# Optimization experiments

Hardware: AMD Instinct MI355X
Metric: run time of the kernel (lower is better)

Reference implementation:

```python
import jax, jax.numpy as jnp
import numpy as np

FACTOR = 5  # routing softmax power


def setup_inputs() -> dict:
    key = jax.random.key(0)
    kq, kk, kv = jax.random.split(key, 3)
    B, L, S, H, E, D = 2, 2048, 2048, 16, 64, 64
    queries = jax.random.normal(kq, (B, L, H, E), dtype=jnp.float32)
    keys = jax.random.normal(kk, (B, S, H, E), dtype=jnp.float32)
    values = jax.random.normal(kv, (B, S, H, D), dtype=jnp.float32)
    return {"queries": queries, "keys": keys, "values": values}


def reference(queries, keys, values):
    # NOTE: original computes scale = 1/sqrt(E) but never applies it; faithful.
    # Original computes the same unscaled QK^T twice; compute once and reuse.
    scores = jnp.einsum('blhe,bshe->bhls', queries, keys)  # [B,H,L,S]
    dense = jax.nn.softmax(scores, axis=-1)
    routing = dense ** FACTOR  # softmax(scores)**factor == routing_scores
    combined = (routing + dense) * 0.5
    sparse = combined / jnp.sum(combined, axis=-1, keepdims=True)
    V = jnp.einsum('bhls,bshd->blhd', sparse, values)  # [B,L,H,D]
    return V
```

## Files before the change

kernel.cpp:

```cpp
#include <hip/hip_runtime.h>
#include <math.h>


typedef _Float16 h8 __attribute__((ext_vector_type(8)));
typedef float f4 __attribute__((ext_vector_type(4)));
typedef float f16v __attribute__((ext_vector_type(16)));
typedef unsigned int u4v __attribute__((ext_vector_type(4)));

constexpr int Sc = 2048, Hc = 16;
constexpr int KB = 64, NT = Sc / KB;
constexpr float LOG2E = 1.4426950408889634f;

__device__ __forceinline__ f16v mm32(h8 a, h8 b, f16v c) {
  return __builtin_amdgcn_mfma_f32_32x32x16_f16(a, b, c, 0, 0, 0);
}
__device__ __forceinline__ unsigned pku(float a, float b) {
  return __builtin_bit_cast(unsigned, __builtin_amdgcn_cvt_pkrtz(a, b));
}

__global__ __launch_bounds__(256, 2) void dsa_mfma(
    const float* __restrict__ Q, const float* __restrict__ K,
    const float* __restrict__ V, float* __restrict__ O) {
  __shared__ __align__(16) _Float16 Ks[2][64 * 64];
  __shared__ __align__(16) _Float16 Vts[2][64 * 64];

  const int tid = threadIdx.x;
  const int w = tid >> 6, lane = tid & 63, lm = lane & 31, hi = lane >> 5;
  const int swz = (lm & 7) << 3;

  const int blk = blockIdx.x;
  const int ww = (blk & 7) * 64 + (blk >> 3);
  const int qtb = ww & 15, bh = ww >> 4;
  const int b = bh >> 4, h = bh & 15;

  const size_t base = ((size_t)b * Sc * Hc + h) * 64;
  const float* Qb = Q + base;
  const float* Kb = K + base;
  const float* Vb = V + base;
  const int q0 = qtb * 128 + w * 32;

  h8 qf[4];
#pragma unroll
  for (int s = 0; s < 4; ++s) {
    const float* p = Qb + (size_t)(q0 + lm) * 1024 + s * 16 + hi * 8;
    f4 a = *(const f4*)p, c = *(const f4*)(p + 4);
#pragma unroll
    for (int i = 0; i < 4; ++i) {
      qf[s][i] = (_Float16)(a[i] * LOG2E);
      qf[s][4 + i] = (_Float16)(c[i] * LOG2E);
    }
  }

  f16v O1[2] = {}, O5[2] = {};
  float mr = -INFINITY, S1 = 0.f, S5 = 0.f;

  f4 kf[4];
  float vreg[2][8];
  const int krow = tid & 63, kq = tid >> 6;
  const int vd = tid & 63, vo0 = (tid >> 6) * 2;

  auto LOADK = [&](int k0) {
#pragma unroll
    for (int j = 0; j < 4; ++j)
      kf[j] = *(const f4*)(Kb + (size_t)(k0 + krow) * 1024 + kq * 16 + 4 * j);
  };
  auto LOADV = [&](int k0) {
#pragma unroll
    for (int i = 0; i < 2; ++i) {
      const float* p = Vb + (size_t)(k0 + (vo0 + i) * 8) * 1024 + vd;
#pragma unroll
      for (int j = 0; j < 8; ++j) vreg[i][j] = p[(size_t)j * 1024];
    }
  };
  auto STORE = [&](int buf) {
#pragma unroll
    for (int i = 0; i < 2; ++i) {
      u4v wv = {pku(kf[2 * i][0], kf[2 * i][1]), pku(kf[2 * i][2], kf[2 * i][3]),
                pku(kf[2 * i + 1][0], kf[2 * i + 1][1]), pku(kf[2 * i + 1][2], kf[2 * i + 1][3])};
      int col = (kq * 16 + 8 * i) ^ ((krow & 7) << 3);
      *(h8*)&Ks[buf][krow * 64 + col] = __builtin_bit_cast(h8, wv);
    }
#pragma unroll
    for (int i = 0; i < 2; ++i) {
      u4v wv = {pku(vreg[i][0], vreg[i][1]), pku(vreg[i][2], vreg[i][3]),
                pku(vreg[i][4], vreg[i][5]), pku(vreg[i][6], vreg[i][7])};
      int col = ((vo0 + i) * 8) ^ ((vd & 7) << 3);
      *(h8*)&Vts[buf][vd * 64 + col] = __builtin_bit_cast(h8, wv);
    }
  };

  LOADK(0);
  LOADV(0);
  STORE(0);
  LOADK(KB);
  LOADV(KB);
  __syncthreads();

#pragma unroll 1
  for (int t = 0; t < NT; ++t) {
    const int cur = t & 1;
    if (t + 1 < NT) STORE(cur ^ 1);
    if (t + 2 < NT) {
      LOADK((t + 2) * KB);
      LOADV((t + 2) * KB);
    }

    f16v sc[2] = {};
    __builtin_amdgcn_s_setprio(1);
#pragma unroll
    for (int s = 0; s < 4; ++s) {
      h8 a0 = *(const h8*)&Ks[cur][lm * 64 + ((s * 16 + hi * 8) ^ swz)];
      h8 a1 = *(const h8*)&Ks[cur][(32 + lm) * 64 + ((s * 16 + hi * 8) ^ swz)];
      sc[0] = mm32(a0, qf[s], sc[0]);
      sc[1] = mm32(a1, qf[s], sc[1]);
    }
    __builtin_amdgcn_s_setprio(0);

    float tm = -INFINITY;
#pragma unroll
    for (int kh = 0; kh < 2; ++kh)
#pragma unroll
      for (int r = 0; r < 16; ++r) tm = fmaxf(tm, sc[kh][r]);
    tm = fmaxf(tm, __shfl_xor(tm, 32));
    if (__any(tm > mr)) {
      float nm = fmaxf(mr, tm);
      float f = __builtin_amdgcn_exp2f(mr - nm);
      float f2 = f * f, f5 = f2 * f2 * f;
      mr = nm;
      S1 *= f;
      S5 *= f5;
#pragma unroll
      for (int dt = 0; dt < 2; ++dt) {
        O1[dt] *= f;
        O5[dt] *= f5;
      }
    }

    float t1 = 0.f, t5 = 0.f;
#pragma unroll
    for (int s = 0; s < 4; ++s) {
      const int kh = s >> 1, s8 = (s & 1) * 8;
      float e[8], e5[8];
#pragma unroll
      for (int j = 0; j < 8; ++j) {
        e[j] = __builtin_amdgcn_exp2f(sc[kh][s8 + j] - mr);
        float e2 = e[j] * e[j];
        e5[j] = e2 * e2 * e[j];
        t1 += e[j];
        t5 += e5[j];
      }
      auto rA = __builtin_amdgcn_permlane32_swap(pku(e[0], e[1]), pku(e[4], e[5]), false, false);
      auto rB = __builtin_amdgcn_permlane32_swap(pku(e[2], e[3]), pku(e[6], e[7]), false, false);
      u4v bwE = {(unsigned)rA[0], (unsigned)rB[0], (unsigned)rA[1], (unsigned)rB[1]};
      h8 bE = __builtin_bit_cast(h8, bwE);
      auto rC = __builtin_amdgcn_permlane32_swap(pku(e5[0], e5[1]), pku(e5[4], e5[5]), false, false);
      auto rD = __builtin_amdgcn_permlane32_swap(pku(e5[2], e5[3]), pku(e5[6], e5[7]), false, false);
      u4v bw5 = {(unsigned)rC[0], (unsigned)rD[0], (unsigned)rC[1], (unsigned)rD[1]};
      h8 b5 = __builtin_bit_cast(h8, bw5);

      h8 v0 = *(const h8*)&Vts[cur][lm * 64 + ((s * 16 + hi * 8) ^ swz)];
      h8 v1 = *(const h8*)&Vts[cur][(32 + lm) * 64 + ((s * 16 + hi * 8) ^ swz)];
      __builtin_amdgcn_s_setprio(1);
      O1[0] = mm32(v0, bE, O1[0]);
      O1[1] = mm32(v1, bE, O1[1]);
      O5[0] = mm32(v0, b5, O5[0]);
      O5[1] = mm32(v1, b5, O5[1]);
      __builtin_amdgcn_s_setprio(0);
    }
    t1 += __shfl_xor(t1, 32);
    t5 += __shfl_xor(t5, 32);
    S1 += t1;
    S5 += t5;

    __syncthreads();
  }

  const float z = S1, z2 = z * z, z4 = z2 * z2;
  const float inv = 1.0f / (S5 + z4 * S1);
#pragma unroll
  for (int dt = 0; dt < 2; ++dt)
#pragma unroll
    for (int i = 0; i < 4; ++i) {
      f4 o;
#pragma unroll
      for (int j = 0; j < 4; ++j)
        o[j] = (O5[dt][4 * i + j] + z4 * O1[dt][4 * i + j]) * inv;
      *(f4*)(O + base + (size_t)(q0 + lm) * 1024 + dt * 32 + 8 * i + 4 * hi) = o;
    }
}

extern "C" void kernel_launch(void* const* d_in, const int* in_sizes, int n_in,
                              void* d_out, int out_size, void* d_ws, size_t ws_size,
                              hipStream_t stream) {
  const float* q = (const float*)d_in[0];
  const float* k = (const float*)d_in[1];
  const float* v = (const float*)d_in[2];
  float* o = (float*)d_out;
  dsa_mfma<<<dim3(512), dim3(256), 0, stream>>>(q, k, v, o);
}
```

Before: 93.15 us.

## Compute row sums via MFMA with ones and fifth power in packed fp16

Replaces the scalar per-element accumulation of the exp and exp^5 row sums with extra MFMA instructions that multiply a ones vector by the probability fragments. The fifth power is now computed after packing, as fp16 vector multiplies, so only one set of permlane swaps is needed. The running-max reduction becomes a tree reduction. This removes VALU work and shuffles but adds two MFMAs per sub-step and computes the fifth power in fp16 instead of fp32, which can underflow or lose precision.

New measurement: 91.35 us. About the same (-1.9%).

```diff
diff --git a/kernel.cpp b/kernel.cpp
--- a/kernel.cpp
+++ b/kernel.cpp
@@ -50,9 +50,13 @@
       qf[s][4 + i] = (_Float16)(c[i] * LOG2E);
     }
   }
+  h8 ones;
+#pragma unroll
+  for (int i = 0; i < 8; ++i) ones[i] = (_Float16)1.0f;
 
   f16v O1[2] = {}, O5[2] = {};
-  float mr = -INFINITY, S1 = 0.f, S5 = 0.f;
+  f16v S1a = {}, S5a = {};
+  float mr = -INFINITY;
 
   f4 kf[4];
   float vreg[2][8];
@@ -116,19 +120,21 @@
     }
     __builtin_amdgcn_s_setprio(0);
 
-    float tm = -INFINITY;
+    float m16[16];
 #pragma unroll
-    for (int kh = 0; kh < 2; ++kh)
+    for (int r = 0; r < 16; ++r) m16[r] = fmaxf(sc[0][r], sc[1][r]);
 #pragma unroll
-      for (int r = 0; r < 16; ++r) tm = fmaxf(tm, sc[kh][r]);
-    tm = fmaxf(tm, __shfl_xor(tm, 32));
+    for (int d = 8; d >= 1; d >>= 1)
+#pragma unroll
+      for (int r = 0; r < d; ++r) m16[r] = fmaxf(m16[r], m16[r + d]);
+    float tm = fmaxf(m16[0], __shfl_xor(m16[0], 32));
     if (__any(tm > mr)) {
       float nm = fmaxf(mr, tm);
       float f = __builtin_amdgcn_exp2f(mr - nm);
       float f2 = f * f, f5 = f2 * f2 * f;
       mr = nm;
-      S1 *= f;
-      S5 *= f5;
+      S1a *= f;
+      S5a *= f5;
 #pragma unroll
       for (int dt = 0; dt < 2; ++dt) {
         O1[dt] *= f;
@@ -136,47 +142,35 @@
       }
     }
 
-    float t1 = 0.f, t5 = 0.f;
 #pragma unroll
     for (int s = 0; s < 4; ++s) {
       const int kh = s >> 1, s8 = (s & 1) * 8;
-      float e[8], e5[8];
+      float e[8];
 #pragma unroll
-      for (int j = 0; j < 8; ++j) {
-        e[j] = __builtin_amdgcn_exp2f(sc[kh][s8 + j] - mr);
-        float e2 = e[j] * e[j];
-        e5[j] = e2 * e2 * e[j];
-        t1 += e[j];
-        t5 += e5[j];
-      }
+      for (int j = 0; j < 8; ++j) e[j] = __builtin_amdgcn_exp2f(sc[kh][s8 + j] - mr);
       auto rA = __builtin_amdgcn_permlane32_swap(pku(e[0], e[1]), pku(e[4], e[5]), false, false);
       auto rB = __builtin_amdgcn_permlane32_swap(pku(e[2], e[3]), pku(e[6], e[7]), false, false);
       u4v bwE = {(unsigned)rA[0], (unsigned)rB[0], (unsigned)rA[1], (unsigned)rB[1]};
       h8 bE = __builtin_bit_cast(h8, bwE);
-      auto rC = __builtin_amdgcn_permlane32_swap(pku(e5[0], e5[1]), pku(e5[4], e5[5]), false, false);
-      auto rD = __builtin_amdgcn_permlane32_swap(pku(e5[2], e5[3]), pku(e5[6], e5[7]), false, false);
-      u4v bw5 = {(unsigned)rC[0], (unsigned)rD[0], (unsigned)rC[1], (unsigned)rD[1]};
-      h8 b5 = __builtin_bit_cast(h8, bw5);
+      h8 b2 = bE * bE, b4 = b2 * b2, b5 = b4 * bE;
 
       h8 v0 = *(const h8*)&Vts[cur][lm * 64 + ((s * 16 + hi * 8) ^ swz)];
       h8 v1 = *(const h8*)&Vts[cur][(32 + lm) * 64 + ((s * 16 + hi * 8) ^ swz)];
       __builtin_amdgcn_s_setprio(1);
       O1[0] = mm32(v0, bE, O1[0]);
       O1[1] = mm32(v1, bE, O1[1]);
+      S1a = mm32(ones, bE, S1a);
       O5[0] = mm32(v0, b5, O5[0]);
       O5[1] = mm32(v1, b5, O5[1]);
+      S5a = mm32(ones, b5, S5a);
       __builtin_amdgcn_s_setprio(0);
     }
-    t1 += __shfl_xor(t1, 32);
-    t5 += __shfl_xor(t5, 32);
-    S1 += t1;
-    S5 += t5;
 
     __syncthreads();
   }
 
-  const float z = S1, z2 = z * z, z4 = z2 * z2;
-  const float inv = 1.0f / (S5 + z4 * S1);
+  const float z = S1a[0], z2 = z * z, z4 = z2 * z2;
+  const float inv = 1.0f / (S5a[0] + z4 * S1a[0]);
 #pragma unroll
   for (int dt = 0; dt < 2; ++dt)
 #pragma unroll
```

## Switch to 16x16 MFMA with 8 waves, LDS-staged P and skippable power-5 path

Applied to the files above, without the earlier changes.

Restructures the flash-style kernel from four waves using 32x32x16 MFMA to eight waves of 16 query rows each using 16x16x32 MFMA. Probabilities now go through a per-wave LDS buffer instead of permlane swaps. The fifth power is computed in packed fp16 and row sums are accumulated with fdot2. The O5 MFMAs and S5 accumulation are skipped for a tile when no row max is within 4.9 of the running max, so that contribution is treated as negligible. This aims to cut MFMA and exp work and raise occupancy, but adds LDS traffic, lowers precision by computing e^5 in fp16, and the skip approximates the sum.

New measurement: 115.2 us. 1.24x slower.

```diff
diff --git a/kernel.cpp b/kernel.cpp
--- a/kernel.cpp
+++ b/kernel.cpp
@@ -3,30 +3,36 @@
 
 
 typedef _Float16 h8 __attribute__((ext_vector_type(8)));
+typedef _Float16 h4 __attribute__((ext_vector_type(4)));
+typedef _Float16 h2 __attribute__((ext_vector_type(2)));
+typedef __fp16 g2 __attribute__((ext_vector_type(2)));
 typedef float f4 __attribute__((ext_vector_type(4)));
-typedef float f16v __attribute__((ext_vector_type(16)));
 typedef unsigned int u4v __attribute__((ext_vector_type(4)));
 
 constexpr int Sc = 2048, Hc = 16;
 constexpr int KB = 64, NT = Sc / KB;
 constexpr float LOG2E = 1.4426950408889634f;
 
-__device__ __forceinline__ f16v mm32(h8 a, h8 b, f16v c) {
-  return __builtin_amdgcn_mfma_f32_32x32x16_f16(a, b, c, 0, 0, 0);
+__device__ __forceinline__ f4 mm16(h8 a, h8 b, f4 c) {
+  return __builtin_amdgcn_mfma_f32_16x16x32_f16(a, b, c, 0, 0, 0);
 }
 __device__ __forceinline__ unsigned pku(float a, float b) {
   return __builtin_bit_cast(unsigned, __builtin_amdgcn_cvt_pkrtz(a, b));
 }
-
-__global__ __launch_bounds__(256, 2) void dsa_mfma(
+__device__ __forceinline__ float fdot2(h2 a, float c) {
+  const g2 one2 = {(__fp16)1.0f, (__fp16)1.0f};
+  return __builtin_amdgcn_fdot2(__builtin_bit_cast(g2, a), one2, c, false);
+}
+
+__global__ __launch_bounds__(512, 2) void dsa_mfma(
     const float* __restrict__ Q, const float* __restrict__ K,
     const float* __restrict__ V, float* __restrict__ O) {
-  __shared__ __align__(16) _Float16 Ks[2][64 * 64];
-  __shared__ __align__(16) _Float16 Vts[2][64 * 64];
+  __shared__ __align__(16) _Float16 kv[2][2][64 * 64];
+  __shared__ __align__(16) _Float16 Ps[8][2][16 * 64];
 
   const int tid = threadIdx.x;
-  const int w = tid >> 6, lane = tid & 63, lm = lane & 31, hi = lane >> 5;
-  const int swz = (lm & 7) << 3;
+  const int w = tid >> 6, lane = tid & 63, lq = lane & 15, lg = lane >> 4;
+  const int kxor = (lq & 7) << 3;
 
   const int blk = blockIdx.x;
   const int ww = (blk & 7) * 64 + (blk >> 3);
@@ -37,56 +43,46 @@
   const float* Qb = Q + base;
   const float* Kb = K + base;
   const float* Vb = V + base;
-  const int q0 = qtb * 128 + w * 32;
-
-  h8 qf[4];
-#pragma unroll
-  for (int s = 0; s < 4; ++s) {
-    const float* p = Qb + (size_t)(q0 + lm) * 1024 + s * 16 + hi * 8;
+  const int q0 = qtb * 128 + w * 16;
+
+  h8 qf[2];
+#pragma unroll
+  for (int ks = 0; ks < 2; ++ks) {
+    const float* p = Qb + (size_t)(q0 + lq) * 1024 + ks * 32 + lg * 8;
     f4 a = *(const f4*)p, c = *(const f4*)(p + 4);
 #pragma unroll
     for (int i = 0; i < 4; ++i) {
-      qf[s][i] = (_Float16)(a[i] * LOG2E);
-      qf[s][4 + i] = (_Float16)(c[i] * LOG2E);
+      qf[ks][i] = (_Float16)(a[i] * LOG2E);
+      qf[ks][4 + i] = (_Float16)(c[i] * LOG2E);
     }
   }
 
-  f16v O1[2] = {}, O5[2] = {};
-  float mr = -INFINITY, S1 = 0.f, S5 = 0.f;
-
-  f4 kf[4];
-  float vreg[2][8];
-  const int krow = tid & 63, kq = tid >> 6;
-  const int vd = tid & 63, vo0 = (tid >> 6) * 2;
-
+  f4 O1[4] = {}, O5[4] = {};
+  float S1p = 0.f, S5p = 0.f, mr = -INFINITY;
+
+  f4 kf[2];
+  float vreg[8];
   auto LOADK = [&](int k0) {
-#pragma unroll
-    for (int j = 0; j < 4; ++j)
-      kf[j] = *(const f4*)(Kb + (size_t)(k0 + krow) * 1024 + kq * 16 + 4 * j);
+    const float* p = Kb + (size_t)(k0 + lane) * 1024 + w * 8;
+    kf[0] = *(const f4*)p;
+    kf[1] = *(const f4*)(p + 4);
   };
   auto LOADV = [&](int k0) {
-#pragma unroll
-    for (int i = 0; i < 2; ++i) {
-      const float* p = Vb + (size_t)(k0 + (vo0 + i) * 8) * 1024 + vd;
-#pragma unroll
-      for (int j = 0; j < 8; ++j) vreg[i][j] = p[(size_t)j * 1024];
-    }
+    const float* p = Vb + (size_t)(k0 + w * 8) * 1024 + lane;
+#pragma unroll
+    for (int j = 0; j < 8; ++j) vreg[j] = p[(size_t)j * 1024];
   };
   auto STORE = [&](int buf) {
-#pragma unroll
-    for (int i = 0; i < 2; ++i) {
-      u4v wv = {pku(kf[2 * i][0], kf[2 * i][1]), pku(kf[2 * i][2], kf[2 * i][3]),
-                pku(kf[2 * i + 1][0], kf[2 * i + 1][1]), pku(kf[2 * i + 1][2], kf[2 * i + 1][3])};
-      int col = (kq * 16 + 8 * i) ^ ((krow & 7) << 3);
-      *(h8*)&Ks[buf][krow * 64 + col] = __builtin_bit_cast(h8, wv);
-    }
-#pragma unroll
-    for (int i = 0; i < 2; ++i) {
-      u4v wv = {pku(vreg[i][0], vreg[i][1]), pku(vreg[i][2], vreg[i][3]),
-                pku(vreg[i][4], vreg[i][5]), pku(vreg[i][6], vreg[i][7])};
-      int col = ((vo0 + i) * 8) ^ ((vd & 7) << 3);
-      *(h8*)&Vts[buf][vd * 64 + col] = __builtin_bit_cast(h8, wv);
-    }
+    _Float16* Ks = &kv[buf][0][0];
+    _Float16* Vts = &kv[buf][1][0];
+    u4v kw = {pku(kf[0][0], kf[0][1]), pku(kf[0][2], kf[0][3]),
+              pku(kf[1][0], kf[1][1]), pku(kf[1][2], kf[1][3])};
+    int kcol = (w * 8) ^ ((lane & 7) << 3);
+    *(h8*)&Ks[lane * 64 + kcol] = __builtin_bit_cast(h8, kw);
+    u4v vw = {pku(vreg[0], vreg[1]), pku(vreg[2], vreg[3]),
+              pku(vreg[4], vreg[5]), pku(vreg[6], vreg[7])};
+    int vcol = (w * 8) ^ ((lane & 7) << 3);
+    *(h8*)&Vts[lane * 64 + vcol] = __builtin_bit_cast(h8, vw);
   };
 
   LOADK(0);
@@ -105,88 +101,104 @@
       LOADV((t + 2) * KB);
     }
 
-    f16v sc[2] = {};
+    const _Float16* Ks = &kv[cur][0][0];
+    f4 sc[4];
+#pragma unroll
+    for (int mt = 0; mt < 4; ++mt) sc[mt] = f4{};
     __builtin_amdgcn_s_setprio(1);
 #pragma unroll
-    for (int s = 0; s < 4; ++s) {
-      h8 a0 = *(const h8*)&Ks[cur][lm * 64 + ((s * 16 + hi * 8) ^ swz)];
-      h8 a1 = *(const h8*)&Ks[cur][(32 + lm) * 64 + ((s * 16 + hi * 8) ^ swz)];
-      sc[0] = mm32(a0, qf[s], sc[0]);
-      sc[1] = mm32(a1, qf[s], sc[1]);
-    }
+    for (int ks = 0; ks < 2; ++ks)
+#pragma unroll
+      for (int mt = 0; mt < 4; ++mt) {
+        h8 a = *(const h8*)&Ks[(mt * 16 + lq) * 64 + ((ks * 32 + lg * 8) ^ kxor)];
+        sc[mt] = mm16(a, qf[ks], sc[mt]);
+      }
     __builtin_amdgcn_s_setprio(0);
 
-    float tm = -INFINITY;
-#pragma unroll
-    for (int kh = 0; kh < 2; ++kh)
-#pragma unroll
-      for (int r = 0; r < 16; ++r) tm = fmaxf(tm, sc[kh][r]);
+    float m4[4];
+#pragma unroll
+    for (int mt = 0; mt < 4; ++mt)
+      m4[mt] = fmaxf(fmaxf(sc[mt][0], sc[mt][1]), fmaxf(sc[mt][2], sc[mt][3]));
+    float tm = fmaxf(fmaxf(m4[0], m4[1]), fmaxf(m4[2], m4[3]));
+    tm = fmaxf(tm, __shfl_xor(tm, 16));
     tm = fmaxf(tm, __shfl_xor(tm, 32));
     if (__any(tm > mr)) {
       float nm = fmaxf(mr, tm);
       float f = __builtin_amdgcn_exp2f(mr - nm);
       float f2 = f * f, f5 = f2 * f2 * f;
       mr = nm;
-      S1 *= f;
-      S5 *= f5;
-#pragma unroll
-      for (int dt = 0; dt < 2; ++dt) {
+      S1p *= f;
+      S5p *= f5;
+#pragma unroll
+      for (int dt = 0; dt < 4; ++dt) {
         O1[dt] *= f;
         O5[dt] *= f5;
       }
     }
-
-    float t1 = 0.f, t5 = 0.f;
-#pragma unroll
-    for (int s = 0; s < 4; ++s) {
-      const int kh = s >> 1, s8 = (s & 1) * 8;
-      float e[8], e5[8];
-#pragma unroll
-      for (int j = 0; j < 8; ++j) {
-        e[j] = __builtin_amdgcn_exp2f(sc[kh][s8 + j] - mr);
-        float e2 = e[j] * e[j];
-        e5[j] = e2 * e2 * e[j];
-        t1 += e[j];
-        t5 += e5[j];
-      }
-      auto rA = __builtin_amdgcn_permlane32_swap(pku(e[0], e[1]), pku(e[4], e[5]), false, false);
-      auto rB = __builtin_amdgcn_permlane32_swap(pku(e[2], e[3]), pku(e[6], e[7]), false, false);
-      u4v bwE = {(unsigned)rA[0], (unsigned)rB[0], (unsigned)rA[1], (unsigned)rB[1]};
-      h8 bE = __builtin_bit_cast(h8, bwE);
-      auto rC = __builtin_amdgcn_permlane32_swap(pku(e5[0], e5[1]), pku(e5[4], e5[5]), false, false);
-      auto rD = __builtin_amdgcn_permlane32_swap(pku(e5[2], e5[3]), pku(e5[6], e5[7]), false, false);
-      u4v bw5 = {(unsigned)rC[0], (unsigned)rD[0], (unsigned)rC[1], (unsigned)rD[1]};
-      h8 b5 = __builtin_bit_cast(h8, bw5);
-
-      h8 v0 = *(const h8*)&Vts[cur][lm * 64 + ((s * 16 + hi * 8) ^ swz)];
-      h8 v1 = *(const h8*)&Vts[cur][(32 + lm) * 64 + ((s * 16 + hi * 8) ^ swz)];
+    const bool do5 = __any(tm > mr - 4.9f);
+
+#pragma unroll
+    for (int mt = 0; mt < 4; ++mt) {
+      float e0 = __builtin_amdgcn_exp2f(sc[mt][0] - mr);
+      float e1 = __builtin_amdgcn_exp2f(sc[mt][1] - mr);
+      float e2 = __builtin_amdgcn_exp2f(sc[mt][2] - mr);
+      float e3 = __builtin_amdgcn_exp2f(sc[mt][3] - mr);
+      h2 a = __builtin_bit_cast(h2, pku(e0, e1));
+      h2 bb = __builtin_bit_cast(h2, pku(e2, e3));
+      h4 pe = {a[0], a[1], bb[0], bb[1]};
+      S1p = fdot2(a, fdot2(bb, S1p));
+      h4 p2 = pe * pe, p4 = p2 * p2, p5 = p4 * pe;
+      int pcol = (mt * 16 + lg * 4) ^ kxor;
+      *(h4*)&Ps[w][0][lq * 64 + pcol] = pe;
+      *(h4*)&Ps[w][1][lq * 64 + pcol] = p5;
+      if (do5) {
+        h2 c = {p5[0], p5[1]}, d = {p5[2], p5[3]};
+        S5p = fdot2(c, fdot2(d, S5p));
+      }
+    }
+
+    const _Float16* Vts = &kv[cur][1][0];
+#pragma unroll
+    for (int ks = 0; ks < 2; ++ks) {
+      const int rc = (ks * 32 + lg * 8) ^ kxor;
+      h8 pb = *(const h8*)&Ps[w][0][lq * 64 + rc];
       __builtin_amdgcn_s_setprio(1);
-      O1[0] = mm32(v0, bE, O1[0]);
-      O1[1] = mm32(v1, bE, O1[1]);
-      O5[0] = mm32(v0, b5, O5[0]);
-      O5[1] = mm32(v1, b5, O5[1]);
+      if (do5) {
+        h8 p5b = *(const h8*)&Ps[w][1][lq * 64 + rc];
+#pragma unroll
+        for (int dt = 0; dt < 4; ++dt) {
+          h8 v = *(const h8*)&Vts[(dt * 16 + lq) * 64 + rc];
+          O1[dt] = mm16(v, pb, O1[dt]);
+          O5[dt] = mm16(v, p5b, O5[dt]);
+        }
+      } else {
+#pragma unroll
+        for (int dt = 0; dt < 4; ++dt) {
+          h8 v = *(const h8*)&Vts[(dt * 16 + lq) * 64 + rc];
+          O1[dt] = mm16(v, pb, O1[dt]);
+        }
+      }
       __builtin_amdgcn_s_setprio(0);
     }
-    t1 += __shfl_xor(t1, 32);
-    t5 += __shfl_xor(t5, 32);
-    S1 += t1;
-    S5 += t5;
 
     __syncthreads();
   }
 
+  float S1 = S1p;
+  S1 += __shfl_xor(S1, 16);
+  S1 += __shfl_xor(S1, 32);
+  float S5 = S5p;
+  S5 += __shfl_xor(S5, 16);
+  S5 += __shfl_xor(S5, 32);
   const float z = S1, z2 = z * z, z4 = z2 * z2;
   const float inv = 1.0f / (S5 + z4 * S1);
 #pragma unroll
-  for (int dt = 0; dt < 2; ++dt)
-#pragma unroll
-    for (int i = 0; i < 4; ++i) {
-      f4 o;
-#pragma unroll
-      for (int j = 0; j < 4; ++j)
-        o[j] = (O5[dt][4 * i + j] + z4 * O1[dt][4 * i + j]) * inv;
-      *(f4*)(O + base + (size_t)(q0 + lm) * 1024 + dt * 32 + 8 * i + 4 * hi) = o;
-    }
+  for (int dt = 0; dt < 4; ++dt) {
+    f4 o;
+#pragma unroll
+    for (int j = 0; j < 4; ++j) o[j] = (O5[dt][j] + z4 * O1[dt][j]) * inv;
+    *(f4*)(O + base + (size_t)(q0 + lq) * 1024 + dt * 16 + lg * 4) = o;
+  }
 }
 
 extern "C" void kernel_launch(void* const* d_in, const int* in_sizes, int n_in,
@@ -196,5 +208,5 @@
   const float* k = (const float*)d_in[1];
   const float* v = (const float*)d_in[2];
   float* o = (float*)d_out;
-  dsa_mfma<<<dim3(512), dim3(256), 0, stream>>>(q, k, v, o);
-}
+  dsa_mfma<<<dim3(512), dim3(512), 0, stream>>>(q, k, v, o);
+}
```
